# Optimization experiments

Measured on AMD Instinct MI355X. Metric: run time of the kernel, lower is better.

## Reference

```python
import jax, jax.numpy as jnp
import numpy as np

HEADS = 16
DIM = 1024


def setup_inputs() -> dict:
    key = jax.random.key(0)
    ks = jax.random.split(key, 9)
    b, n, d = 2, 2048, DIM
    scale = 1.0 / np.sqrt(d)  # xavier-ish scale for weights
    x = jax.random.normal(ks[0], (b, n, d), dtype=jnp.float32)
    Wq = jax.random.normal(ks[1], (d, d), dtype=jnp.float32) * scale
    Wk = jax.random.normal(ks[2], (d, d), dtype=jnp.float32) * scale
    Wv = jax.random.normal(ks[3], (d, d), dtype=jnp.float32) * scale
    Wo = jax.random.normal(ks[4], (d, d), dtype=jnp.float32) * scale
    bq = jnp.zeros((d,), jnp.float32)
    bk = jnp.zeros((d,), jnp.float32)
    bv = jnp.zeros((d,), jnp.float32)
    bo = jnp.zeros((d,), jnp.float32)
    return {"x": x, "Wq": Wq, "bq": bq, "Wk": Wk, "bk": bk,
            "Wv": Wv, "bv": bv, "Wo": Wo, "bo": bo}


def reference(x, Wq, bq, Wk, bk, Wv, bv, Wo, bo):
    b, n, d = x.shape
    h = HEADS
    hd = d // h
    # torch Linear: y = x @ W.T + b  (W stored [out, in]; here square so W given as [d,d])
    q = x @ Wq.T + bq
    k = x @ Wk.T + bk
    v = x @ Wv.T + bv
    # b n (h d) -> b h n d
    q = q.reshape(b, n, h, hd).transpose(0, 2, 1, 3)
    k = k.reshape(b, n, h, hd).transpose(0, 2, 1, 3)
    v = v.reshape(b, n, h, hd).transpose(0, 2, 1, 3)
    # NOTE: scale is 1/sqrt(dim), not 1/sqrt(head_dim), faithful to source.
    scores = jnp.einsum('bhqd,bhkd->bhqk', q, k) / jnp.sqrt(jnp.float32(d))
    attn = jax.nn.softmax(scores, axis=-1)
    out = jnp.einsum('bhqk,bhkd->bhqd', attn, v)
    out = out.transpose(0, 2, 1, 3).reshape(b, n, d)  # b h n d -> b n (h d)
    return out @ Wo.T + bo
```

## Files before the change

kernel.cpp:

```cpp
#include <hip/hip_runtime.h>

typedef unsigned short u16t;
typedef __attribute__((ext_vector_type(8))) short bf16x8;
typedef __attribute__((ext_vector_type(4))) float f32x4;

#define DM   1024
#define SEQL 2048
#define NHD  16
#define HDD  64

#define GLL16(g, l) __builtin_amdgcn_global_load_lds( \
    (const __attribute__((address_space(1))) void*)(g), \
    (__attribute__((address_space(3))) void*)(l), 16, 0, 0)

#if defined(__has_builtin)
#if __has_builtin(__builtin_amdgcn_exp2f)
#define EXP2(x) __builtin_amdgcn_exp2f(x)
#else
#define EXP2(x) exp2f(x)
#endif
#else
#define EXP2(x) exp2f(x)
#endif

__device__ __forceinline__ u16t f2bf(float f) {
  unsigned u = __float_as_uint(f);
  return (u16t)((u + 0x7fffu + ((u >> 16) & 1u)) >> 16);
}
__device__ __forceinline__ unsigned pack_bf16_2(float a, float b) {
  const unsigned ua = __float_as_uint(a) + 0x8000u;
  const unsigned ub = __float_as_uint(b) + 0x8000u;
  return __builtin_amdgcn_perm(ub, ua, 0x07060302);
}

struct ConvArgs { const float* src[5]; u16t* dst[5]; };

__global__ __launch_bounds__(256) void conv_kernel(ConvArgs a) {
  const int gid = blockIdx.x * 256 + threadIdx.x;
  const int e = gid << 2;
  int sel, off;
  if (e < 4194304) { sel = 0; off = e; }
  else { const int r = e - 4194304; sel = 1 + (r >> 20); off = r & 1048575; }
  const float4 f = *(const float4*)(a.src[sel] + off);
  union { u16t s[4]; uint2 u; } o;
  o.s[0] = f2bf(f.x); o.s[1] = f2bf(f.y); o.s[2] = f2bf(f.z); o.s[3] = f2bf(f.w);
  *(uint2*)(a.dst[sel] + off) = o.u;
}

__device__ __forceinline__ int gslot(int m, int kc) { return (m << 2) + (kc ^ ((m >> 1) & 3)); }

template<int MODE>
__device__ __forceinline__ void qkv_body(
    const u16t* __restrict__ X, const u16t* __restrict__ W,
    const float* __restrict__ bias, float oscale, u16t* __restrict__ outB,
    u16t* smem)
{
  u16t* const Es = smem;

  const int tid = threadIdx.x;
  const int l = tid & 63, w = tid >> 6, q = l >> 4, ln = l & 15;
  const int trow0 = blockIdx.y << 7;
  const int dcol0 = blockIdx.x << 7;
  const int wm = (w >> 1) << 6, wn = (w & 1) << 6;

  const int s0 = (w << 6) + l, s1 = s0 + 256;
  const int m0 = s0 >> 2, kc0 = (s0 & 3) ^ ((m0 >> 1) & 3);
  const int m1 = s1 >> 2, kc1 = (s1 & 3) ^ ((m1 >> 1) & 3);
  const u16t* gA0 = X + (size_t)(trow0 + m0) * DM + (kc0 << 3);
  const u16t* gA1 = X + (size_t)(trow0 + m1) * DM + (kc1 << 3);
  const u16t* gB0 = W + (size_t)(dcol0 + m0) * DM + (kc0 << 3);
  const u16t* gB1 = W + (size_t)(dcol0 + m1) * DM + (kc1 << 3);
  const int dO0 = (w << 6) << 3;
  const int dO1 = ((w << 6) + 256) << 3;

  f32x4 acc[4][4] = {};

  GLL16(gA0, smem + dO0);
  GLL16(gA1, smem + dO1);
  GLL16(gB0, smem + 4096 + dO0);
  GLL16(gB1, smem + 4096 + dO1);

  for (int kt = 0; kt < DM; kt += 32) {
    const int it = kt >> 5;
    u16t* const curA = smem + ((it & 1) ? 8192 : 0);
    u16t* const curB = curA + 4096;
    __syncthreads();
    if (kt + 32 < DM) {
      u16t* const nA = smem + ((it & 1) ? 0 : 8192);
      u16t* const nB = nA + 4096;
      GLL16(gA0 + kt + 32, nA + dO0);
      GLL16(gA1 + kt + 32, nA + dO1);
      GLL16(gB0 + kt + 32, nB + dO0);
      GLL16(gB1 + kt + 32, nB + dO1);
    }

    bf16x8 af[4], bfr[4];
    #pragma unroll
    for (int mi = 0; mi < 4; ++mi) {
      const int r = wm + (mi << 4) + ln;
      af[mi] = *(const bf16x8*)&((MODE == 1 ? curB : curA)[gslot(r, q) << 3]);
    }
    #pragma unroll
    for (int ni = 0; ni < 4; ++ni) {
      const int r = wn + (ni << 4) + ln;
      bfr[ni] = *(const bf16x8*)&((MODE == 1 ? curA : curB)[gslot(r, q) << 3]);
    }
    #pragma unroll
    for (int mi = 0; mi < 4; ++mi)
      #pragma unroll
      for (int ni = 0; ni < 4; ++ni)
        acc[mi][ni] = __builtin_amdgcn_mfma_f32_16x16x32_bf16(af[mi], bfr[ni], acc[mi][ni], 0, 0, 0);
  }

  __syncthreads();

  if (MODE == 1) {
    #pragma unroll
    for (int mi = 0; mi < 4; ++mi) {
      const int dl = wm + (mi << 4) + (q << 2);
      const float4 b4 = *(const float4*)&bias[dcol0 + dl];
      #pragma unroll
      for (int ni = 0; ni < 4; ++ni) {
        const int tl = wn + (ni << 4) + ln;
        uint2 pk;
        pk.x = pack_bf16_2((acc[mi][ni][0] + b4.x) * oscale, (acc[mi][ni][1] + b4.y) * oscale);
        pk.y = pack_bf16_2((acc[mi][ni][2] + b4.z) * oscale, (acc[mi][ni][3] + b4.w) * oscale);
        *(uint2*)&Es[tl * 136 + dl] = pk;
      }
    }
    __syncthreads();
    #pragma unroll
    for (int it = 0; it < 8; ++it) {
      const int u = (it << 8) + tid;
      const int tl = u >> 4, c8 = u & 15;
      const uint4 vv = *(const uint4*)&Es[tl * 136 + (c8 << 3)];
      const int tok = trow0 + tl;
      const int b = tok >> 11, n = tok & (SEQL - 1);
      const int dg = dcol0 + (c8 << 3);
      const int h = dg >> 6, hd = dg & 63;
      *(uint4*)&outB[((size_t)(b * NHD + h) * SEQL + n) * HDD + hd] = vv;
    }
  } else {
    #pragma unroll
    for (int ni = 0; ni < 4; ++ni) {
      const int dl = wn + (ni << 4) + ln;
      const float bv = bias[dcol0 + dl];
      #pragma unroll
      for (int mi = 0; mi < 4; ++mi) {
        const int g = (wm >> 2) + (mi << 2) + q;
        const int g6 = g & 15;
        const int gp = (g & 16) | (g6 & 8) | ((g6 & 3) << 1) | ((g6 >> 2) & 1);
        uint2 pk;
        pk.x = pack_bf16_2(acc[mi][ni][0] + bv, acc[mi][ni][1] + bv);
        pk.y = pack_bf16_2(acc[mi][ni][2] + bv, acc[mi][ni][3] + bv);
        *(uint2*)&Es[dl * 136 + (gp << 2)] = pk;
      }
    }
    __syncthreads();
    #pragma unroll
    for (int it = 0; it < 8; ++it) {
      const int u = (it << 8) + tid;
      const int dl = u >> 4, c8 = u & 15;
      const uint4 vv = *(const uint4*)&Es[dl * 136 + (c8 << 3)];
      const int dg = dcol0 + dl;
      const int h = dg >> 6, hd = dg & 63;
      const int b = trow0 >> 11;
      const int n = (trow0 & (SEQL - 1)) + (c8 << 3);
      *(uint4*)&outB[((size_t)(b * NHD + h) * HDD + hd) * SEQL + n] = vv;
    }
  }
}

struct QKVArgs { const u16t* W[3]; const float* b[3]; u16t* dst[3]; };

__global__ __launch_bounds__(256) void qkv_kernel(const u16t* __restrict__ X, QKVArgs g) {
  __shared__ alignas(16) u16t smem[17408];
  const int z = blockIdx.z;
  if (z == 2)      qkv_body<2>(X, g.W[2], g.b[2], 1.0f, g.dst[2], smem);
  else if (z == 1) qkv_body<1>(X, g.W[1], g.b[1], 1.0f, g.dst[1], smem);
  else             qkv_body<1>(X, g.W[0], g.b[0], 0.04508422f, g.dst[0], smem);
}

__global__ __launch_bounds__(256, 4) void attn_kernel(
    const u16t* __restrict__ Qb, const u16t* __restrict__ Kb,
    const u16t* __restrict__ Vt, u16t* __restrict__ ctx)
{
  __shared__ alignas(16) u16t smem[16384];

  const int tid = threadIdx.x;
  const int l = tid & 63, w = tid >> 6;
  const int q = l >> 4, ln = l & 15;
  const int bh = blockIdx.x, q0 = blockIdx.y << 7;
  const size_t hb = (size_t)bh * SEQL * HDD;
  const u16t* Qg = Qb + hb;
  const u16t* Kg = Kb + hb;
  const u16t* Vg = Vt + hb;

  bf16x8 qf[2][2];
  #pragma unroll
  for (int g = 0; g < 2; ++g) {
    const int qr = q0 + (w << 5) + (g << 4) + ln;
    #pragma unroll
    for (int ks = 0; ks < 2; ++ks)
      qf[g][ks] = *(const bf16x8*)(Qg + (size_t)qr * HDD + (((ks << 2) + q) << 3));
  }

  const int u0 = tid,       r0 = u0 >> 3, c0 = (u0 & 7) ^ (r0 & 7);
  const int u1 = 256 + tid, r1 = u1 >> 3, c1 = (u1 & 7) ^ (r1 & 7);
  const u16t* const kS0 = Kg + (size_t)r0 * HDD + (c0 << 3);
  const u16t* const kS1 = Kg + (size_t)r1 * HDD + (c1 << 3);
  const u16t* const vS0 = Vg + (size_t)r0 * SEQL + (c0 << 3);
  const u16t* const vS1 = Vg + (size_t)r1 * SEQL + (c1 << 3);
  const int dK0 = (w << 6) << 3, dK1 = (256 + (w << 6)) << 3;

  GLL16(kS0, smem + dK0);
  GLL16(kS1, smem + dK1);
  GLL16(vS0, smem + 4096 + dK0);
  GLL16(vS1, smem + 4096 + dK1);

  const short one_s = (short)0x3F80;
  const bf16x8 ones = { one_s, one_s, one_s, one_s, one_s, one_s, one_s, one_s };

  f32x4 accO[2][4] = {};
  f32x4 accL[2] = {};

  for (int t = 0; t < 32; ++t) {
    const int cb = (t & 1) ? 8192 : 0;
    u16t* const Ks = smem + cb;
    u16t* const Vs = smem + cb + 4096;
    __syncthreads();
    if (t + 1 < 32) {
      const int nb = (t & 1) ? 0 : 8192;
      const int ko = (t + 1) << 6;
      GLL16(kS0 + (size_t)ko * HDD, smem + nb + dK0);
      GLL16(kS1 + (size_t)ko * HDD, smem + nb + dK1);
      GLL16(vS0 + ko, smem + nb + 4096 + dK0);
      GLL16(vS1 + ko, smem + nb + 4096 + dK1);
    }

    f32x4 sc[2][4] = {{}, {}};
    #pragma unroll
    for (int ks = 0; ks < 2; ++ks) {
      const int hc = (ks << 2) + q;
      #pragma unroll
      for (int ni = 0; ni < 4; ++ni) {
        const int kr = (ni << 4) + ln;
        const bf16x8 ak = *(const bf16x8*)&Ks[((kr << 3) + (hc ^ (kr & 7))) << 3];
        #pragma unroll
        for (int g = 0; g < 2; ++g)
          sc[g][ni] = __builtin_amdgcn_mfma_f32_16x16x32_bf16(ak, qf[g][ks], sc[g][ni], 0, 0, 0);
      }
    }

    unsigned pk01[2][4], pk23[2][4];
    #pragma unroll
    for (int g = 0; g < 2; ++g)
      #pragma unroll
      for (int ni = 0; ni < 4; ++ni) {
        const float e0 = EXP2(sc[g][ni][0]);
        const float e1 = EXP2(sc[g][ni][1]);
        const float e2 = EXP2(sc[g][ni][2]);
        const float e3 = EXP2(sc[g][ni][3]);
        pk01[g][ni] = pack_bf16_2(e0, e1);
        pk23[g][ni] = pack_bf16_2(e2, e3);
      }

    #pragma unroll
    for (int ks = 0; ks < 2; ++ks) {
      union { unsigned u[4]; bf16x8 v; } bfv[2];
      #pragma unroll
      for (int g = 0; g < 2; ++g) {
        bfv[g].u[0] = pk01[g][(ks << 1) + 0];
        bfv[g].u[1] = pk23[g][(ks << 1) + 0];
        bfv[g].u[2] = pk01[g][(ks << 1) + 1];
        bfv[g].u[3] = pk23[g][(ks << 1) + 1];
      }
      #pragma unroll
      for (int g = 0; g < 2; ++g)
        accL[g] = __builtin_amdgcn_mfma_f32_16x16x32_bf16(ones, bfv[g].v, accL[g], 0, 0, 0);
      const int c = (ks << 2) + q;
      #pragma unroll
      for (int nio = 0; nio < 4; ++nio) {
        const int vr = (nio << 4) + ln;
        const bf16x8 av = *(const bf16x8*)&Vs[((vr << 3) + (c ^ (vr & 7))) << 3];
        #pragma unroll
        for (int g = 0; g < 2; ++g)
          accO[g][nio] = __builtin_amdgcn_mfma_f32_16x16x32_bf16(av, bfv[g].v, accO[g][nio], 0, 0, 0);
      }
    }
  }

  __syncthreads();
  #pragma unroll
  for (int g = 0; g < 2; ++g) {
    const float inv = 1.0f / accL[g][0];
    const int tl = (w << 5) + (g << 4) + ln;
    #pragma unroll
    for (int nio = 0; nio < 4; ++nio) {
      uint2 pk;
      pk.x = pack_bf16_2(accO[g][nio][0] * inv, accO[g][nio][1] * inv);
      pk.y = pack_bf16_2(accO[g][nio][2] * inv, accO[g][nio][3] * inv);
      *(uint2*)&smem[tl * 72 + (nio << 4) + (q << 2)] = pk;
    }
  }
  __syncthreads();
  const int h = bh & (NHD - 1), bi = bh >> 4;
  #pragma unroll
  for (int it = 0; it < 4; ++it) {
    const int u = (it << 8) + tid;
    const int tl = u >> 3, c8 = u & 7;
    const uint4 vv = *(const uint4*)&smem[tl * 72 + (c8 << 3)];
    *(uint4*)&ctx[((size_t)(bi * SEQL + q0 + tl)) * DM + (h << 6) + (c8 << 3)] = vv;
  }
}

__global__ __launch_bounds__(256) void outproj_kernel(
    const u16t* __restrict__ A, const u16t* __restrict__ W,
    const float* __restrict__ bias, float* __restrict__ outF)
{
  __shared__ alignas(16) u16t smem[24576];

  const int tid = threadIdx.x;
  const int l = tid & 63, w = tid >> 6, q = l >> 4, ln = l & 15;
  const int row0 = blockIdx.y << 7;
  const int col0 = blockIdx.x << 6;
  const int wm = (w >> 1) << 6, wn = (w & 1) << 5;

  const u16t* gA[4]; const u16t* gB[2];
  int dA[4], dB[2];
  #pragma unroll
  for (int p = 0; p < 4; ++p) {
    const int s = tid + (p << 8);
    const int m = s >> 3, kc = (s & 7) ^ (m & 7);
    gA[p] = A + (size_t)(row0 + m) * DM + (kc << 3);
    dA[p] = s << 3;
  }
  #pragma unroll
  for (int p = 0; p < 2; ++p) {
    const int s = tid + (p << 8);
    const int m = s >> 3, kc = (s & 7) ^ (m & 7);
    gB[p] = W + (size_t)(col0 + m) * DM + (kc << 3);
    dB[p] = s << 3;
  }

  f32x4 acc[4][2] = {};

  #pragma unroll
  for (int p = 0; p < 4; ++p) GLL16(gA[p], smem + dA[p]);
  #pragma unroll
  for (int p = 0; p < 2; ++p) GLL16(gB[p], smem + 8192 + dB[p]);

  for (int t = 0; t < 16; ++t) {
    u16t* const curA = smem + ((t & 1) ? 12288 : 0);
    u16t* const curB = smem + ((t & 1) ? 20480 : 8192);
    __syncthreads();
    if (t + 1 < 16) {
      u16t* const nA = smem + ((t & 1) ? 0 : 12288);
      u16t* const nB = smem + ((t & 1) ? 8192 : 20480);
      const int kt = (t + 1) << 6;
      #pragma unroll
      for (int p = 0; p < 4; ++p) GLL16(gA[p] + kt, nA + dA[p]);
      #pragma unroll
      for (int p = 0; p < 2; ++p) GLL16(gB[p] + kt, nB + dB[p]);
    }

    #pragma unroll
    for (int ks = 0; ks < 2; ++ks) {
      const int hc = (ks << 2) + q;
      bf16x8 af[4], bfr[2];
      #pragma unroll
      for (int mi = 0; mi < 4; ++mi) {
        const int r = wm + (mi << 4) + ln;
        af[mi] = *(const bf16x8*)&curA[((r << 3) + (hc ^ (r & 7))) << 3];
      }
      #pragma unroll
      for (int ni = 0; ni < 2; ++ni) {
        const int r = wn + (ni << 4) + ln;
        bfr[ni] = *(const bf16x8*)&curB[((r << 3) + (hc ^ (r & 7))) << 3];
      }
      #pragma unroll
      for (int mi = 0; mi < 4; ++mi)
        #pragma unroll
        for (int ni = 0; ni < 2; ++ni)
          acc[mi][ni] = __builtin_amdgcn_mfma_f32_16x16x32_bf16(af[mi], bfr[ni], acc[mi][ni], 0, 0, 0);
    }
  }

  #pragma unroll
  for (int ni = 0; ni < 2; ++ni) {
    const int col = col0 + wn + (ni << 4) + ln;
    const float bv = bias[col];
    #pragma unroll
    for (int mi = 0; mi < 4; ++mi)
      #pragma unroll
      for (int r = 0; r < 4; ++r) {
        const int row = row0 + wm + (mi << 4) + (q << 2) + r;
        outF[(size_t)row * DM + col] = acc[mi][ni][r] + bv;
      }
  }
}

extern "C" void kernel_launch(void* const* d_in, const int* in_sizes, int n_in,
                              void* d_out, int out_size, void* d_ws, size_t ws_size,
                              hipStream_t stream)
{
  const float* x  = (const float*)d_in[0];
  const float* Wq = (const float*)d_in[1];
  const float* bq = (const float*)d_in[2];
  const float* Wk = (const float*)d_in[3];
  const float* bk = (const float*)d_in[4];
  const float* Wv = (const float*)d_in[5];
  const float* bv = (const float*)d_in[6];
  const float* Wo = (const float*)d_in[7];
  const float* bo = (const float*)d_in[8];
  float* out = (float*)d_out;

  u16t* p = (u16t*)d_ws;
  u16t* xb  = p;  p += 4194304;
  u16t* Wqb = p;  p += 1048576;
  u16t* Wkb = p;  p += 1048576;
  u16t* Wvb = p;  p += 1048576;
  u16t* Wob = p;  p += 1048576;
  u16t* Qbf = p;  p += 4194304;
  u16t* Kbf = p;  p += 4194304;
  u16t* Vtb = p;  p += 4194304;
  u16t* ctx = p;  p += 4194304;

  ConvArgs ca;
  ca.src[0] = x;  ca.dst[0] = xb;
  ca.src[1] = Wq; ca.dst[1] = Wqb;
  ca.src[2] = Wk; ca.dst[2] = Wkb;
  ca.src[3] = Wv; ca.dst[3] = Wvb;
  ca.src[4] = Wo; ca.dst[4] = Wob;
  conv_kernel<<<8192, 256, 0, stream>>>(ca);

  QKVArgs qa;
  qa.W[0] = Wqb; qa.W[1] = Wkb; qa.W[2] = Wvb;
  qa.b[0] = bq;  qa.b[1] = bk;  qa.b[2] = bv;
  qa.dst[0] = Qbf; qa.dst[1] = Kbf; qa.dst[2] = Vtb;
  qkv_kernel<<<dim3(8, 32, 3), 256, 0, stream>>>(xb, qa);

  attn_kernel<<<dim3(32, 16), 256, 0, stream>>>(Qbf, Kbf, Vtb, ctx);

  outproj_kernel<<<dim3(16, 32), 256, 0, stream>>>(ctx, Wob, bo, out);
}
```

Measured before the change: 174.4 us.

## Retile QKV projection GEMM to 128x64 blocks with 64-wide K steps

The QKV projection kernel now computes 128-token by 64-feature tiles instead of 128x128, which doubles the grid to 1536 blocks. It also takes K steps of 64 with a new 8-chunk XOR swizzle and an inner two-substep loop. Each block covers exactly one head, so the epilogue address math is simpler. The aim is more blocks in flight across the CUs and half as many barriers per K pass. The cost is lower arithmetic intensity per block and a larger LDS footprint (48KB), which may limit occupancy.

```diff
diff --git a/kernel.cpp b/kernel.cpp
--- a/kernel.cpp
+++ b/kernel.cpp
@@ -47,8 +47,6 @@
   *(uint2*)(a.dst[sel] + off) = o.u;
 }
 
-__device__ __forceinline__ int gslot(int m, int kc) { return (m << 2) + (kc ^ ((m >> 1) & 3)); }
-
 template<int MODE>
 __device__ __forceinline__ void qkv_body(
     const u16t* __restrict__ X, const u16t* __restrict__ W,
@@ -60,93 +58,107 @@
   const int tid = threadIdx.x;
   const int l = tid & 63, w = tid >> 6, q = l >> 4, ln = l & 15;
   const int trow0 = blockIdx.y << 7;
-  const int dcol0 = blockIdx.x << 7;
-  const int wm = (w >> 1) << 6, wn = (w & 1) << 6;
-
-  const int s0 = (w << 6) + l, s1 = s0 + 256;
-  const int m0 = s0 >> 2, kc0 = (s0 & 3) ^ ((m0 >> 1) & 3);
-  const int m1 = s1 >> 2, kc1 = (s1 & 3) ^ ((m1 >> 1) & 3);
-  const u16t* gA0 = X + (size_t)(trow0 + m0) * DM + (kc0 << 3);
-  const u16t* gA1 = X + (size_t)(trow0 + m1) * DM + (kc1 << 3);
-  const u16t* gB0 = W + (size_t)(dcol0 + m0) * DM + (kc0 << 3);
-  const u16t* gB1 = W + (size_t)(dcol0 + m1) * DM + (kc1 << 3);
-  const int dO0 = (w << 6) << 3;
-  const int dO1 = ((w << 6) + 256) << 3;
-
-  f32x4 acc[4][4] = {};
-
-  GLL16(gA0, smem + dO0);
-  GLL16(gA1, smem + dO1);
-  GLL16(gB0, smem + 4096 + dO0);
-  GLL16(gB1, smem + 4096 + dO1);
-
-  for (int kt = 0; kt < DM; kt += 32) {
-    const int it = kt >> 5;
-    u16t* const curA = smem + ((it & 1) ? 8192 : 0);
-    u16t* const curB = curA + 4096;
+  const int dcol0 = blockIdx.x << 6;
+
+  constexpr int MI = (MODE == 1) ? 2 : 4;
+  constexpr int NI = (MODE == 1) ? 4 : 2;
+  const int wm = (MODE == 1) ? ((w >> 1) << 5) : ((w >> 1) << 6);
+  const int wn = (MODE == 1) ? ((w & 1) << 6) : ((w & 1) << 5);
+
+  const u16t* gA[4]; const u16t* gB[2];
+  int dA[4], dB[2];
+  #pragma unroll
+  for (int p = 0; p < 4; ++p) {
+    const int s = tid + (p << 8);
+    const int m = s >> 3, kc = (s & 7) ^ (m & 7);
+    gA[p] = X + (size_t)(trow0 + m) * DM + (kc << 3);
+    dA[p] = s << 3;
+  }
+  #pragma unroll
+  for (int p = 0; p < 2; ++p) {
+    const int s = tid + (p << 8);
+    const int m = s >> 3, kc = (s & 7) ^ (m & 7);
+    gB[p] = W + (size_t)(dcol0 + m) * DM + (kc << 3);
+    dB[p] = s << 3;
+  }
+
+  f32x4 acc[MI][NI] = {};
+
+  #pragma unroll
+  for (int p = 0; p < 4; ++p) GLL16(gA[p], smem + dA[p]);
+  #pragma unroll
+  for (int p = 0; p < 2; ++p) GLL16(gB[p], smem + 8192 + dB[p]);
+
+  for (int t = 0; t < 16; ++t) {
+    u16t* const curA = smem + ((t & 1) ? 12288 : 0);
+    u16t* const curB = smem + ((t & 1) ? 20480 : 8192);
     __syncthreads();
-    if (kt + 32 < DM) {
-      u16t* const nA = smem + ((it & 1) ? 0 : 8192);
-      u16t* const nB = nA + 4096;
-      GLL16(gA0 + kt + 32, nA + dO0);
-      GLL16(gA1 + kt + 32, nA + dO1);
-      GLL16(gB0 + kt + 32, nB + dO0);
-      GLL16(gB1 + kt + 32, nB + dO1);
-    }
-
-    bf16x8 af[4], bfr[4];
-    #pragma unroll
-    for (int mi = 0; mi < 4; ++mi) {
-      const int r = wm + (mi << 4) + ln;
-      af[mi] = *(const bf16x8*)&((MODE == 1 ? curB : curA)[gslot(r, q) << 3]);
-    }
-    #pragma unroll
-    for (int ni = 0; ni < 4; ++ni) {
-      const int r = wn + (ni << 4) + ln;
-      bfr[ni] = *(const bf16x8*)&((MODE == 1 ? curA : curB)[gslot(r, q) << 3]);
-    }
-    #pragma unroll
-    for (int mi = 0; mi < 4; ++mi)
-      #pragma unroll
-      for (int ni = 0; ni < 4; ++ni)
-        acc[mi][ni] = __builtin_amdgcn_mfma_f32_16x16x32_bf16(af[mi], bfr[ni], acc[mi][ni], 0, 0, 0);
+    if (t + 1 < 16) {
+      u16t* const nA = smem + ((t & 1) ? 0 : 12288);
+      u16t* const nB = smem + ((t & 1) ? 8192 : 20480);
+      const int kt = (t + 1) << 6;
+      #pragma unroll
+      for (int p = 0; p < 4; ++p) GLL16(gA[p] + kt, nA + dA[p]);
+      #pragma unroll
+      for (int p = 0; p < 2; ++p) GLL16(gB[p] + kt, nB + dB[p]);
+    }
+
+    #pragma unroll
+    for (int ks = 0; ks < 2; ++ks) {
+      const int hc = (ks << 2) + q;
+      bf16x8 af[MI], bfr[NI];
+      #pragma unroll
+      for (int mi = 0; mi < MI; ++mi) {
+        const int r = wm + (mi << 4) + ln;
+        af[mi] = *(const bf16x8*)&((MODE == 1 ? curB : curA)[((r << 3) + (hc ^ (r & 7))) << 3]);
+      }
+      #pragma unroll
+      for (int ni = 0; ni < NI; ++ni) {
+        const int r = wn + (ni << 4) + ln;
+        bfr[ni] = *(const bf16x8*)&((MODE == 1 ? curA : curB)[((r << 3) + (hc ^ (r & 7))) << 3]);
+      }
+      #pragma unroll
+      for (int mi = 0; mi < MI; ++mi)
+        #pragma unroll
+        for (int ni = 0; ni < NI; ++ni)
+          acc[mi][ni] = __builtin_amdgcn_mfma_f32_16x16x32_bf16(af[mi], bfr[ni], acc[mi][ni], 0, 0, 0);
+    }
   }
 
   __syncthreads();
+  const int h = dcol0 >> 6;
 
   if (MODE == 1) {
     #pragma unroll
-    for (int mi = 0; mi < 4; ++mi) {
+    for (int mi = 0; mi < MI; ++mi) {
       const int dl = wm + (mi << 4) + (q << 2);
       const float4 b4 = *(const float4*)&bias[dcol0 + dl];
       #pragma unroll
-      for (int ni = 0; ni < 4; ++ni) {
+      for (int ni = 0; ni < NI; ++ni) {
         const int tl = wn + (ni << 4) + ln;
         uint2 pk;
         pk.x = pack_bf16_2((acc[mi][ni][0] + b4.x) * oscale, (acc[mi][ni][1] + b4.y) * oscale);
         pk.y = pack_bf16_2((acc[mi][ni][2] + b4.z) * oscale, (acc[mi][ni][3] + b4.w) * oscale);
-        *(uint2*)&Es[tl * 136 + dl] = pk;
+        *(uint2*)&Es[tl * 72 + dl] = pk;
       }
     }
     __syncthreads();
     #pragma unroll
-    for (int it = 0; it < 8; ++it) {
+    for (int it = 0; it < 4; ++it) {
       const int u = (it << 8) + tid;
-      const int tl = u >> 4, c8 = u & 15;
-      const uint4 vv = *(const uint4*)&Es[tl * 136 + (c8 << 3)];
+      const int tl = u >> 3, c8 = u & 7;
+      const uint4 vv = *(const uint4*)&Es[tl * 72 + (c8 << 3)];
       const int tok = trow0 + tl;
       const int b = tok >> 11, n = tok & (SEQL - 1);
-      const int dg = dcol0 + (c8 << 3);
-      const int h = dg >> 6, hd = dg & 63;
-      *(uint4*)&outB[((size_t)(b * NHD + h) * SEQL + n) * HDD + hd] = vv;
+      *(uint4*)&outB[((size_t)(b * NHD + h) * SEQL + n) * HDD + (c8 << 3)] = vv;
     }
   } else {
     #pragma unroll
-    for (int ni = 0; ni < 4; ++ni) {
+    for (int ni = 0; ni < NI; ++ni) {
       const int dl = wn + (ni << 4) + ln;
       const float bv = bias[dcol0 + dl];
       #pragma unroll
-      for (int mi = 0; mi < 4; ++mi) {
+      for (int mi = 0; mi < MI; ++mi) {
         const int g = (wm >> 2) + (mi << 2) + q;
         const int g6 = g & 15;
         const int gp = (g & 16) | (g6 & 8) | ((g6 & 3) << 1) | ((g6 >> 2) & 1);
@@ -157,16 +169,14 @@
       }
     }
     __syncthreads();
-    #pragma unroll
-    for (int it = 0; it < 8; ++it) {
+    const int b = trow0 >> 11;
+    #pragma unroll
+    for (int it = 0; it < 4; ++it) {
       const int u = (it << 8) + tid;
       const int dl = u >> 4, c8 = u & 15;
       const uint4 vv = *(const uint4*)&Es[dl * 136 + (c8 << 3)];
-      const int dg = dcol0 + dl;
-      const int h = dg >> 6, hd = dg & 63;
-      const int b = trow0 >> 11;
       const int n = (trow0 & (SEQL - 1)) + (c8 << 3);
-      *(uint4*)&outB[((size_t)(b * NHD + h) * HDD + hd) * SEQL + n] = vv;
+      *(uint4*)&outB[((size_t)(b * NHD + h) * HDD + dl) * SEQL + n] = vv;
     }
   }
 }
@@ -174,7 +184,7 @@
 struct QKVArgs { const u16t* W[3]; const float* b[3]; u16t* dst[3]; };
 
 __global__ __launch_bounds__(256) void qkv_kernel(const u16t* __restrict__ X, QKVArgs g) {
-  __shared__ alignas(16) u16t smem[17408];
+  __shared__ alignas(16) u16t smem[24576];
   const int z = blockIdx.z;
   if (z == 2)      qkv_body<2>(X, g.W[2], g.b[2], 1.0f, g.dst[2], smem);
   else if (z == 1) qkv_body<1>(X, g.W[1], g.b[1], 1.0f, g.dst[1], smem);
@@ -438,7 +448,7 @@
   qa.W[0] = Wqb; qa.W[1] = Wkb; qa.W[2] = Wvb;
   qa.b[0] = bq;  qa.b[1] = bk;  qa.b[2] = bv;
   qa.dst[0] = Qbf; qa.dst[1] = Kbf; qa.dst[2] = Vtb;
-  qkv_kernel<<<dim3(8, 32, 3), 256, 0, stream>>>(xb, qa);
+  qkv_kernel<<<dim3(16, 32, 3), 256, 0, stream>>>(xb, qa);
 
   attn_kernel<<<dim3(32, 16), 256, 0, stream>>>(Qbf, Kbf, Vtb, ctx);
 
```

Result: no change. 177.5 us (+1.8%).
